# Optimization experiments

Hardware: AMD Instinct MI355X
Metric: run time of the kernel (lower is better)

## Reference

```python
import jax, jax.numpy as jnp
import numpy as np

SPARSITY_RATIO = 0.1


def setup_inputs() -> dict:
    key = jax.random.key(0)
    ks = jax.random.split(key, 11)
    B, S, d = 4, 2048, 16  # d = n_sparse_dims + 2
    inp = {
        "full": jax.random.normal(ks[0], (B, S, d), dtype=jnp.float32),
        "sw1": jax.random.normal(ks[1], (d, 32), dtype=jnp.float32) * 0.1,
        "sb1": jax.random.normal(ks[2], (32,), dtype=jnp.float32) * 0.1,
        "sw2": jax.random.normal(ks[3], (32, 1), dtype=jnp.float32) * 0.1,
        "sb2": jax.random.normal(ks[4], (1,), dtype=jnp.float32) * 0.1,
        "mw1": jax.random.normal(ks[5], (3 * d, 64), dtype=jnp.float32) * 0.1,
        "mb1": jax.random.normal(ks[6], (64,), dtype=jnp.float32) * 0.1,
        "mw2": jax.random.normal(ks[7], (64, 32), dtype=jnp.float32) * 0.1,
        "mb2": jax.random.normal(ks[8], (32,), dtype=jnp.float32) * 0.1,
        "mw3": jax.random.normal(ks[9], (32, d), dtype=jnp.float32) * 0.1,
        "mb3": jax.random.normal(ks[10], (d,), dtype=jnp.float32) * 0.1,
    }
    return inp


def reference(full, sw1, sb1, sw2, sb2, mw1, mb1, mw2, mb2, mw3, mb3):
    B, S, d = full.shape
    k = max(1, int(S * SPARSITY_RATIO))  # static python int

    # importance scores: Linear(d,32) -> ReLU -> Linear(32,1)
    scores = (jax.nn.relu(full @ sw1 + sb1) @ sw2 + sb2)[..., 0]  # [B, S]
    _, top_idx = jax.lax.top_k(scores, k)  # [B, k]

    # gather selected tokens (keys == values)
    sel = jnp.take_along_axis(full, top_idx[:, :, None], axis=1)  # [B, k, d]

    # First MLP layer on concat([q, keys, values]) decomposed to avoid the
    # [B,S,k,3d] concat: mw1 splits into query / key / value blocks.
    w_q, w_k, w_v = mw1[:d], mw1[d:2 * d], mw1[2 * d:]
    q_part = full @ w_q                     # [B, S, 64]
    kv_part = sel @ (w_k + w_v)             # [B, k, 64]
    h1 = jax.nn.relu(q_part[:, :, None, :] + kv_part[:, None, :, :] + mb1)  # [B,S,k,64]
    h2 = jax.nn.relu(h1 @ mw2 + mb2)        # [B, S, k, 32]
    out = h2 @ mw3 + mb3                    # [B, S, k, d]
    return out.mean(axis=2)                 # [B, S, d]
```

## Files before the change

kernel.cpp:

```cpp
#include <hip/hip_runtime.h>
#include <hip/hip_bf16.h>

#define BB 4
#define SS 2048
#define DD 16
#define KK 204
#define JSPLIT 8

typedef __attribute__((ext_vector_type(8))) short short8;
typedef __attribute__((ext_vector_type(4))) float f32x4;

__device__ inline short f2bf(float x) {
  __hip_bfloat16 b = __float2bfloat16(x);
  return *reinterpret_cast<short*>(&b);
}

__global__ void __launch_bounds__(128) score_kernel(
    const float* __restrict__ full, const float* __restrict__ sw1,
    const float* __restrict__ sb1, const float* __restrict__ sw2,
    const float* __restrict__ sb2, float* __restrict__ scores_g) {
  __shared__ float swT[32][16];
  __shared__ float sb1s[32], sw2s[32];
  int t = threadIdx.x;
#pragma unroll
  for (int it = 0; it < 4; it++) {
    int idx = t + it * 128;
    int n = idx & 31, k = idx >> 5;
    swT[n][k] = sw1[k * 32 + n];
  }
  if (t < 32) { sb1s[t] = sb1[t]; sw2s[t] = sw2[t]; }

  int row = blockIdx.x * 128 + t;
  const float* xp = full + row * DD;
  f32x4 x0 = *(const f32x4*)(xp);
  f32x4 x1 = *(const f32x4*)(xp + 4);
  f32x4 x2 = *(const f32x4*)(xp + 8);
  f32x4 x3 = *(const f32x4*)(xp + 12);
  __syncthreads();

  float sc = sb2[0];
#pragma unroll
  for (int n = 0; n < 32; n++) {
    const f32x4* wp = (const f32x4*)&swT[n][0];
    f32x4 w0 = wp[0], w1 = wp[1], w2 = wp[2], w3 = wp[3];
    float a = sb1s[n];
#pragma unroll
    for (int k = 0; k < 4; k++) a += x0[k] * w0[k];
#pragma unroll
    for (int k = 0; k < 4; k++) a += x1[k] * w1[k];
#pragma unroll
    for (int k = 0; k < 4; k++) a += x2[k] * w2[k];
#pragma unroll
    for (int k = 0; k < 4; k++) a += x3[k] * w3[k];
    sc += fmaxf(a, 0.f) * sw2s[n];
  }
  scores_g[row] = sc;
}

__global__ void __launch_bounds__(1024) select_kernel(
    const float* __restrict__ scores_g, int* __restrict__ s_idx_g) {
  int b = blockIdx.x;
  int t = threadIdx.x;
  int l = t & 63, w = t >> 6;

  __shared__ int hist[2048];
  __shared__ int wtot[16];
  __shared__ unsigned long long s_pfx;
  __shared__ int s_r;

  unsigned long long key[2];
#pragma unroll
  for (int e = 0; e < 2; e++) {
    int i = t + e * 1024;
    unsigned u = __float_as_uint(scores_g[b * SS + i]);
    u = (u & 0x80000000u) ? ~u : (u | 0x80000000u);
    key[e] = ((unsigned long long)u << 11) | (unsigned)(SS - 1 - i);
  }
  if (t == 0) { s_pfx = 0ull; s_r = KK; }

  for (int pass = 0; pass < 4; pass++) {
    int s = 33 - pass * 11;
    hist[t] = 0;
    hist[t + 1024] = 0;
    __syncthreads();
    unsigned long long pfx = s_pfx;
    int r = s_r;
#pragma unroll
    for (int e = 0; e < 2; e++)
      if ((key[e] >> (s + 11)) == pfx)
        atomicAdd(&hist[(int)((key[e] >> s) & 0x7FF)], 1);
    __syncthreads();
    int loc0 = hist[2 * t], loc1 = hist[2 * t + 1];
    int ls0 = loc0 + loc1, ls1 = loc1;
    int tot = ls0;
    int incl = tot;
#pragma unroll
    for (int off = 1; off < 64; off <<= 1) {
      int o = __shfl_down(incl, off);
      incl += (l + off < 64) ? o : 0;
    }
    if (l == 0) wtot[w] = incl;
    __syncthreads();
    int waveoff = 0;
    for (int ww = w + 1; ww < 16; ww++) waveoff += wtot[ww];
    int excl = waveoff + (incl - tot);
    int sufs0 = ls0 + excl, sufs1 = ls1 + excl;
    if (sufs0 >= r && sufs1 < r) {
      s_pfx = (pfx << 11) | (unsigned)(2 * t);
      s_r = r - sufs1;
    }
    if (sufs1 >= r && excl < r) {
      s_pfx = (pfx << 11) | (unsigned)(2 * t + 1);
      s_r = r - excl;
    }
    __syncthreads();
  }

  unsigned long long kstar = s_pfx;
  bool sel0 = (key[0] >= kstar), sel1 = (key[1] >= kstar);
  int c = (sel0 ? 1 : 0) + (sel1 ? 1 : 0);
  int p = c;
#pragma unroll
  for (int off = 1; off < 64; off <<= 1) {
    int o = __shfl_up(p, off);
    p += (l >= off) ? o : 0;
  }
  if (l == 63) wtot[w] = p;
  __syncthreads();
  int base = 0;
  for (int ww = 0; ww < w; ww++) base += wtot[ww];
  int pos = base + p - c;
  if (sel0) s_idx_g[b * KK + pos++] = t;
  if (sel1) s_idx_g[b * KK + pos] = t + 1024;
}

__global__ void __launch_bounds__(512) main_mfma_kernel(
    const float* __restrict__ full, const float* __restrict__ mw1,
    const float* __restrict__ mb1, const float* __restrict__ mw2,
    const float* __restrict__ mb2, const float* __restrict__ mw3,
    const float* __restrict__ mb3, const int* __restrict__ s_idx_g,
    float* __restrict__ out) {
  int mtile = blockIdx.x;
  int bs_base = mtile * 16;
  int b = bs_base >> 11;
  int t = threadIdx.x;
  int w = t >> 6;
  int l = t & 63;
  int ml = l & 15;
  int g = l >> 4;

  __shared__ float s_kvb[KK * 64];
  __shared__ float qs[16 * 64];
  __shared__ float xs[16 * 16];
  __shared__ float s_xsel[KK * DD];
  __shared__ int s_idx[KK];
  float (*red)[512] = (float(*)[512])s_kvb;

  if (t < KK) s_idx[t] = s_idx_g[b * KK + t];
  if (t < 256) xs[t] = full[bs_base * DD + t];
  __syncthreads();

  for (int i = t; i < KK * DD; i += 512)
    s_xsel[i] = full[(b * SS + s_idx[i >> 4]) * DD + (i & 15)];
  float wreg[16];
#pragma unroll
  for (int k = 0; k < 16; k++)
    wreg[k] = mw1[(16 + k) * 64 + l] + mw1[(32 + k) * 64 + l];
  float biasv = mb1[l];

  {
    int r = t >> 5, n = t & 31;
    float q0 = 0.f, q1 = 0.f;
#pragma unroll
    for (int k = 0; k < 16; k++) {
      float xv = xs[r * 16 + k];
      q0 += xv * mw1[k * 64 + n];
      q1 += xv * mw1[k * 64 + n + 32];
    }
    qs[r * 64 + n] = q0;
    qs[r * 64 + n + 32] = q1;
  }
  __syncthreads();

  for (int j = w; j < KK; j += 8) {
    const float* xr = s_xsel + j * DD;
    float a = biasv;
#pragma unroll
    for (int k = 0; k < 16; k++) a += xr[k] * wreg[k];
    s_kvb[j * 64 + l] = a;
  }

  short8 bfrag[2][2];
#pragma unroll
  for (int nt = 0; nt < 2; nt++)
#pragma unroll
    for (int kh = 0; kh < 2; kh++)
#pragma unroll
      for (int i = 0; i < 8; i++) {
        int k = kh * 32 + 8 * g + i;
        bfrag[nt][kh][i] = f2bf(mw2[k * 32 + nt * 16 + ml]);
      }
  f32x4 biasfrag[2];
#pragma unroll
  for (int nt = 0; nt < 2; nt++) {
    float bv = mb2[nt * 16 + ml];
    f32x4 bf;
    bf[0] = bv; bf[1] = bv; bf[2] = bv; bf[3] = bv;
    biasfrag[nt] = bf;
  }
  f32x4 qv[2][2];
  {
    const float* qp = qs + ml * 64 + 8 * g;
    qv[0][0] = *(const f32x4*)(qp);
    qv[0][1] = *(const f32x4*)(qp + 4);
    qv[1][0] = *(const f32x4*)(qp + 32);
    qv[1][1] = *(const f32x4*)(qp + 36);
  }
  __syncthreads();

  float accs[2][4] = {};
  int jbeg = w * 26;
  int jend = jbeg + 26;
  if (jend > KK) jend = KK;
  const float* kvbl = s_kvb + 8 * g;
#pragma unroll 2
  for (int j = jbeg; j < jend; j++) {
    const float* kp = kvbl + j * 64;
    f32x4 kv[2][2];
    kv[0][0] = *(const f32x4*)(kp);
    kv[0][1] = *(const f32x4*)(kp + 4);
    kv[1][0] = *(const f32x4*)(kp + 32);
    kv[1][1] = *(const f32x4*)(kp + 36);

    short8 afrag[2];
#pragma unroll
    for (int kh = 0; kh < 2; kh++)
#pragma unroll
      for (int hf = 0; hf < 2; hf++)
#pragma unroll
        for (int i = 0; i < 4; i++) {
          float h = fmaxf(qv[kh][hf][i] + kv[kh][hf][i], 0.f);
          afrag[kh][hf * 4 + i] = f2bf(h);
        }

#pragma unroll
    for (int nt = 0; nt < 2; nt++) {
      f32x4 c = __builtin_amdgcn_mfma_f32_16x16x32_bf16(
          afrag[0], bfrag[nt][0], biasfrag[nt], 0, 0, 0);
      c = __builtin_amdgcn_mfma_f32_16x16x32_bf16(
          afrag[1], bfrag[nt][1], c, 0, 0, 0);
#pragma unroll
      for (int r = 0; r < 4; r++) accs[nt][r] += fmaxf(c[r], 0.f);
    }
  }

  __syncthreads();
#pragma unroll
  for (int nt = 0; nt < 2; nt++)
#pragma unroll
    for (int r = 0; r < 4; r++)
      red[w][(4 * g + r) * 32 + nt * 16 + ml] = accs[nt][r];
  __syncthreads();
  float sum = 0.f;
#pragma unroll
  for (int ww = 0; ww < JSPLIT; ww++) sum += red[ww][t];
  sum *= (1.0f / (float)KK);
  red[0][t] = sum;
  __syncthreads();

  if (t < 256) {
    int m = t >> 4, dc = t & 15;
    float o = mb3[dc];
#pragma unroll
    for (int n = 0; n < 32; n++) o += red[0][m * 32 + n] * mw3[n * 16 + dc];
    out[(bs_base + m) * 16 + dc] = o;
  }
}

extern "C" void kernel_launch(void* const* d_in, const int* in_sizes, int n_in,
                              void* d_out, int out_size, void* d_ws, size_t ws_size,
                              hipStream_t stream) {
  const float* full = (const float*)d_in[0];
  const float* sw1  = (const float*)d_in[1];
  const float* sb1  = (const float*)d_in[2];
  const float* sw2  = (const float*)d_in[3];
  const float* sb2  = (const float*)d_in[4];
  const float* mw1  = (const float*)d_in[5];
  const float* mb1  = (const float*)d_in[6];
  const float* mw2  = (const float*)d_in[7];
  const float* mb2  = (const float*)d_in[8];
  const float* mw3  = (const float*)d_in[9];
  const float* mb3  = (const float*)d_in[10];
  float* out = (float*)d_out;

  float* scores_g = (float*)d_ws;
  int*   s_idx_g  = (int*)(scores_g + BB * SS);

  score_kernel<<<64, 128, 0, stream>>>(full, sw1, sb1, sw2, sb2, scores_g);
  select_kernel<<<BB, 1024, 0, stream>>>(scores_g, s_idx_g);
  main_mfma_kernel<<<BB * SS / 16, 512, 0, stream>>>(full, mw1, mb1, mw2, mb2,
                                                     mw3, mb3, s_idx_g, out);
}
```

Measured before the change: 40.89 us.

## Fuse scoring into top-k kernel and precompute key/value projections once per batch

New measurement: 47.00 us. +15.0%, slower.

```diff
diff --git a/kernel.cpp b/kernel.cpp
--- a/kernel.cpp
+++ b/kernel.cpp
@@ -15,68 +15,59 @@
   return *reinterpret_cast<short*>(&b);
 }
 
-__global__ void __launch_bounds__(128) score_kernel(
+__global__ void __launch_bounds__(1024) topk_kvb_kernel(
     const float* __restrict__ full, const float* __restrict__ sw1,
     const float* __restrict__ sb1, const float* __restrict__ sw2,
-    const float* __restrict__ sb2, float* __restrict__ scores_g) {
-  __shared__ float swT[32][16];
-  __shared__ float sb1s[32], sw2s[32];
-  int t = threadIdx.x;
-#pragma unroll
-  for (int it = 0; it < 4; it++) {
-    int idx = t + it * 128;
-    int n = idx & 31, k = idx >> 5;
-    swT[n][k] = sw1[k * 32 + n];
-  }
-  if (t < 32) { sb1s[t] = sb1[t]; sw2s[t] = sw2[t]; }
-
-  int row = blockIdx.x * 128 + t;
-  const float* xp = full + row * DD;
-  f32x4 x0 = *(const f32x4*)(xp);
-  f32x4 x1 = *(const f32x4*)(xp + 4);
-  f32x4 x2 = *(const f32x4*)(xp + 8);
-  f32x4 x3 = *(const f32x4*)(xp + 12);
-  __syncthreads();
-
-  float sc = sb2[0];
-#pragma unroll
-  for (int n = 0; n < 32; n++) {
-    const f32x4* wp = (const f32x4*)&swT[n][0];
-    f32x4 w0 = wp[0], w1 = wp[1], w2 = wp[2], w3 = wp[3];
-    float a = sb1s[n];
-#pragma unroll
-    for (int k = 0; k < 4; k++) a += x0[k] * w0[k];
-#pragma unroll
-    for (int k = 0; k < 4; k++) a += x1[k] * w1[k];
-#pragma unroll
-    for (int k = 0; k < 4; k++) a += x2[k] * w2[k];
-#pragma unroll
-    for (int k = 0; k < 4; k++) a += x3[k] * w3[k];
-    sc += fmaxf(a, 0.f) * sw2s[n];
-  }
-  scores_g[row] = sc;
-}
-
-__global__ void __launch_bounds__(1024) select_kernel(
-    const float* __restrict__ scores_g, int* __restrict__ s_idx_g) {
+    const float* __restrict__ sb2, const float* __restrict__ mw1,
+    const float* __restrict__ mb1, float* __restrict__ kvb_g) {
   int b = blockIdx.x;
   int t = threadIdx.x;
   int l = t & 63, w = t >> 6;
 
+  __shared__ float swT[32][16];
+  __shared__ float sb1s[32], sw2s[32];
   __shared__ int hist[2048];
   __shared__ int wtot[16];
   __shared__ unsigned long long s_pfx;
   __shared__ int s_r;
-
+  __shared__ int s_idx[KK];
+  __shared__ float s_x[KK * DD];
+
+  if (t < 512) { int n = t & 31, k = t >> 5; swT[n][k] = sw1[k * 32 + n]; }
+  if (t < 32) { sb1s[t] = sb1[t]; sw2s[t] = sw2[t]; }
+  if (t == 0) { s_pfx = 0ull; s_r = KK; }
+  __syncthreads();
+
+  float sb2v = sb2[0];
   unsigned long long key[2];
 #pragma unroll
   for (int e = 0; e < 2; e++) {
     int i = t + e * 1024;
-    unsigned u = __float_as_uint(scores_g[b * SS + i]);
+    const float* xp = full + (b * SS + i) * DD;
+    f32x4 x0 = *(const f32x4*)(xp);
+    f32x4 x1 = *(const f32x4*)(xp + 4);
+    f32x4 x2 = *(const f32x4*)(xp + 8);
+    f32x4 x3 = *(const f32x4*)(xp + 12);
+    float sc = sb2v;
+#pragma unroll
+    for (int n = 0; n < 32; n++) {
+      const f32x4* wp = (const f32x4*)&swT[n][0];
+      f32x4 w0 = wp[0], w1 = wp[1], w2 = wp[2], w3 = wp[3];
+      float a = sb1s[n];
+#pragma unroll
+      for (int k = 0; k < 4; k++) a += x0[k] * w0[k];
+#pragma unroll
+      for (int k = 0; k < 4; k++) a += x1[k] * w1[k];
+#pragma unroll
+      for (int k = 0; k < 4; k++) a += x2[k] * w2[k];
+#pragma unroll
+      for (int k = 0; k < 4; k++) a += x3[k] * w3[k];
+      sc += fmaxf(a, 0.f) * sw2s[n];
+    }
+    unsigned u = __float_as_uint(sc);
     u = (u & 0x80000000u) ? ~u : (u | 0x80000000u);
     key[e] = ((unsigned long long)u << 11) | (unsigned)(SS - 1 - i);
   }
-  if (t == 0) { s_pfx = 0ull; s_r = KK; }
 
   for (int pass = 0; pass < 4; pass++) {
     int s = 33 - pass * 11;
@@ -130,16 +121,32 @@
   int base = 0;
   for (int ww = 0; ww < w; ww++) base += wtot[ww];
   int pos = base + p - c;
-  if (sel0) s_idx_g[b * KK + pos++] = t;
-  if (sel1) s_idx_g[b * KK + pos] = t + 1024;
+  if (sel0) s_idx[pos++] = t;
+  if (sel1) s_idx[pos] = t + 1024;
+  __syncthreads();
+
+  for (int i = t; i < KK * DD; i += 1024)
+    s_x[i] = full[(b * SS + s_idx[i >> 4]) * DD + (i & 15)];
+  float wreg[16];
+#pragma unroll
+  for (int k = 0; k < 16; k++)
+    wreg[k] = mw1[(16 + k) * 64 + l] + mw1[(32 + k) * 64 + l];
+  float biasv = mb1[l];
+  __syncthreads();
+  for (int j = w; j < KK; j += 16) {
+    const float* xr = s_x + j * DD;
+    float a = biasv;
+#pragma unroll
+    for (int k = 0; k < 16; k++) a += xr[k] * wreg[k];
+    kvb_g[(b * KK + j) * 64 + l] = a;
+  }
 }
 
 __global__ void __launch_bounds__(512) main_mfma_kernel(
     const float* __restrict__ full, const float* __restrict__ mw1,
-    const float* __restrict__ mb1, const float* __restrict__ mw2,
-    const float* __restrict__ mb2, const float* __restrict__ mw3,
-    const float* __restrict__ mb3, const int* __restrict__ s_idx_g,
-    float* __restrict__ out) {
+    const float* __restrict__ mw2, const float* __restrict__ mb2,
+    const float* __restrict__ mw3, const float* __restrict__ mb3,
+    const float* __restrict__ kvb_g, float* __restrict__ out) {
   int mtile = blockIdx.x;
   int bs_base = mtile * 16;
   int b = bs_base >> 11;
@@ -152,21 +159,15 @@
   __shared__ float s_kvb[KK * 64];
   __shared__ float qs[16 * 64];
   __shared__ float xs[16 * 16];
-  __shared__ float s_xsel[KK * DD];
-  __shared__ int s_idx[KK];
   float (*red)[512] = (float(*)[512])s_kvb;
 
-  if (t < KK) s_idx[t] = s_idx_g[b * KK + t];
+  {
+    const f32x4* src = (const f32x4*)(kvb_g + b * KK * 64);
+    f32x4* dst = (f32x4*)s_kvb;
+    for (int i = t; i < KK * 16; i += 512) dst[i] = src[i];
+  }
   if (t < 256) xs[t] = full[bs_base * DD + t];
   __syncthreads();
-
-  for (int i = t; i < KK * DD; i += 512)
-    s_xsel[i] = full[(b * SS + s_idx[i >> 4]) * DD + (i & 15)];
-  float wreg[16];
-#pragma unroll
-  for (int k = 0; k < 16; k++)
-    wreg[k] = mw1[(16 + k) * 64 + l] + mw1[(32 + k) * 64 + l];
-  float biasv = mb1[l];
 
   {
     int r = t >> 5, n = t & 31;
@@ -179,15 +180,6 @@
     }
     qs[r * 64 + n] = q0;
     qs[r * 64 + n + 32] = q1;
-  }
-  __syncthreads();
-
-  for (int j = w; j < KK; j += 8) {
-    const float* xr = s_xsel + j * DD;
-    float a = biasv;
-#pragma unroll
-    for (int k = 0; k < 16; k++) a += xr[k] * wreg[k];
-    s_kvb[j * 64 + l] = a;
   }
 
   short8 bfrag[2][2];
@@ -208,6 +200,8 @@
     bf[0] = bv; bf[1] = bv; bf[2] = bv; bf[3] = bv;
     biasfrag[nt] = bf;
   }
+  __syncthreads();
+
   f32x4 qv[2][2];
   {
     const float* qp = qs + ml * 64 + 8 * g;
@@ -216,7 +210,6 @@
     qv[1][0] = *(const f32x4*)(qp + 32);
     qv[1][1] = *(const f32x4*)(qp + 36);
   }
-  __syncthreads();
 
   float accs[2][4] = {};
   int jbeg = w * 26;
@@ -293,11 +286,10 @@
   const float* mb3  = (const float*)d_in[10];
   float* out = (float*)d_out;
 
-  float* scores_g = (float*)d_ws;
-  int*   s_idx_g  = (int*)(scores_g + BB * SS);
-
-  score_kernel<<<64, 128, 0, stream>>>(full, sw1, sb1, sw2, sb2, scores_g);
-  select_kernel<<<BB, 1024, 0, stream>>>(scores_g, s_idx_g);
-  main_mfma_kernel<<<BB * SS / 16, 512, 0, stream>>>(full, mw1, mb1, mw2, mb2,
-                                                     mw3, mb3, s_idx_g, out);
-}
+  float* kvb_g = (float*)d_ws;
+
+  topk_kvb_kernel<<<BB, 1024, 0, stream>>>(full, sw1, sb1, sw2, sb2, mw1, mb1,
+                                           kvb_g);
+  main_mfma_kernel<<<BB * SS / 16, 512, 0, stream>>>(full, mw1, mw2, mb2, mw3,
+                                                     mb3, kvb_g, out);
+}
```

## Fuse top-k selection into main kernel, redundantly per block

Applied to the files above, without the earlier changes.

Result: faster. 38.84 us (-5.0%).

```diff
diff --git a/kernel.cpp b/kernel.cpp
--- a/kernel.cpp
+++ b/kernel.cpp
@@ -57,88 +57,11 @@
   scores_g[row] = sc;
 }
 
-__global__ void __launch_bounds__(1024) select_kernel(
-    const float* __restrict__ scores_g, int* __restrict__ s_idx_g) {
-  int b = blockIdx.x;
-  int t = threadIdx.x;
-  int l = t & 63, w = t >> 6;
-
-  __shared__ int hist[2048];
-  __shared__ int wtot[16];
-  __shared__ unsigned long long s_pfx;
-  __shared__ int s_r;
-
-  unsigned long long key[2];
-#pragma unroll
-  for (int e = 0; e < 2; e++) {
-    int i = t + e * 1024;
-    unsigned u = __float_as_uint(scores_g[b * SS + i]);
-    u = (u & 0x80000000u) ? ~u : (u | 0x80000000u);
-    key[e] = ((unsigned long long)u << 11) | (unsigned)(SS - 1 - i);
-  }
-  if (t == 0) { s_pfx = 0ull; s_r = KK; }
-
-  for (int pass = 0; pass < 4; pass++) {
-    int s = 33 - pass * 11;
-    hist[t] = 0;
-    hist[t + 1024] = 0;
-    __syncthreads();
-    unsigned long long pfx = s_pfx;
-    int r = s_r;
-#pragma unroll
-    for (int e = 0; e < 2; e++)
-      if ((key[e] >> (s + 11)) == pfx)
-        atomicAdd(&hist[(int)((key[e] >> s) & 0x7FF)], 1);
-    __syncthreads();
-    int loc0 = hist[2 * t], loc1 = hist[2 * t + 1];
-    int ls0 = loc0 + loc1, ls1 = loc1;
-    int tot = ls0;
-    int incl = tot;
-#pragma unroll
-    for (int off = 1; off < 64; off <<= 1) {
-      int o = __shfl_down(incl, off);
-      incl += (l + off < 64) ? o : 0;
-    }
-    if (l == 0) wtot[w] = incl;
-    __syncthreads();
-    int waveoff = 0;
-    for (int ww = w + 1; ww < 16; ww++) waveoff += wtot[ww];
-    int excl = waveoff + (incl - tot);
-    int sufs0 = ls0 + excl, sufs1 = ls1 + excl;
-    if (sufs0 >= r && sufs1 < r) {
-      s_pfx = (pfx << 11) | (unsigned)(2 * t);
-      s_r = r - sufs1;
-    }
-    if (sufs1 >= r && excl < r) {
-      s_pfx = (pfx << 11) | (unsigned)(2 * t + 1);
-      s_r = r - excl;
-    }
-    __syncthreads();
-  }
-
-  unsigned long long kstar = s_pfx;
-  bool sel0 = (key[0] >= kstar), sel1 = (key[1] >= kstar);
-  int c = (sel0 ? 1 : 0) + (sel1 ? 1 : 0);
-  int p = c;
-#pragma unroll
-  for (int off = 1; off < 64; off <<= 1) {
-    int o = __shfl_up(p, off);
-    p += (l >= off) ? o : 0;
-  }
-  if (l == 63) wtot[w] = p;
-  __syncthreads();
-  int base = 0;
-  for (int ww = 0; ww < w; ww++) base += wtot[ww];
-  int pos = base + p - c;
-  if (sel0) s_idx_g[b * KK + pos++] = t;
-  if (sel1) s_idx_g[b * KK + pos] = t + 1024;
-}
-
-__global__ void __launch_bounds__(512) main_mfma_kernel(
+__global__ void __launch_bounds__(512) mega_kernel(
     const float* __restrict__ full, const float* __restrict__ mw1,
     const float* __restrict__ mb1, const float* __restrict__ mw2,
     const float* __restrict__ mb2, const float* __restrict__ mw3,
-    const float* __restrict__ mb3, const int* __restrict__ s_idx_g,
+    const float* __restrict__ mb3, const float* __restrict__ scores_g,
     float* __restrict__ out) {
   int mtile = blockIdx.x;
   int bs_base = mtile * 16;
@@ -154,10 +77,86 @@
   __shared__ float xs[16 * 16];
   __shared__ float s_xsel[KK * DD];
   __shared__ int s_idx[KK];
+  __shared__ int wtot[8];
+  __shared__ unsigned long long s_pfx;
+  __shared__ int s_r;
+  int* hist = (int*)s_kvb;
   float (*red)[512] = (float(*)[512])s_kvb;
 
-  if (t < KK) s_idx[t] = s_idx_g[b * KK + t];
+  unsigned long long key[4];
+#pragma unroll
+  for (int e = 0; e < 4; e++) {
+    int i = t + e * 512;
+    unsigned u = __float_as_uint(scores_g[b * SS + i]);
+    u = (u & 0x80000000u) ? ~u : (u | 0x80000000u);
+    key[e] = ((unsigned long long)u << 11) | (unsigned)(SS - 1 - i);
+  }
   if (t < 256) xs[t] = full[bs_base * DD + t];
+  if (t == 0) { s_pfx = 0ull; s_r = KK; }
+
+  for (int pass = 0; pass < 4; pass++) {
+    int s = 33 - pass * 11;
+#pragma unroll
+    for (int z = 0; z < 4; z++) hist[t * 4 + z] = 0;
+    __syncthreads();
+    unsigned long long pfx = s_pfx;
+    int r = s_r;
+#pragma unroll
+    for (int e = 0; e < 4; e++)
+      if ((key[e] >> (s + 11)) == pfx)
+        atomicAdd(&hist[(int)((key[e] >> s) & 0x7FF)], 1);
+    __syncthreads();
+    int loc[4], ls[5];
+#pragma unroll
+    for (int i2 = 0; i2 < 4; i2++) loc[i2] = hist[t * 4 + i2];
+    ls[4] = 0;
+#pragma unroll
+    for (int i2 = 3; i2 >= 0; i2--) ls[i2] = ls[i2 + 1] + loc[i2];
+    int tot = ls[0];
+    int incl = tot;
+#pragma unroll
+    for (int off = 1; off < 64; off <<= 1) {
+      int o = __shfl_down(incl, off);
+      incl += (l + off < 64) ? o : 0;
+    }
+    if (l == 0) wtot[w] = incl;
+    __syncthreads();
+    int waveoff = 0;
+    for (int ww = w + 1; ww < 8; ww++) waveoff += wtot[ww];
+    int excl = waveoff + (incl - tot);
+#pragma unroll
+    for (int i2 = 0; i2 < 4; i2++) {
+      int sufs = ls[i2] + excl, sufn = ls[i2 + 1] + excl;
+      if (sufs >= r && sufn < r) {
+        s_pfx = (pfx << 11) | (unsigned)(t * 4 + i2);
+        s_r = r - sufn;
+      }
+    }
+    __syncthreads();
+  }
+
+  unsigned long long kstar = s_pfx;
+  bool selm[4];
+  int c = 0;
+#pragma unroll
+  for (int e = 0; e < 4; e++) {
+    selm[e] = (key[e] >= kstar);
+    c += selm[e] ? 1 : 0;
+  }
+  int p = c;
+#pragma unroll
+  for (int off = 1; off < 64; off <<= 1) {
+    int o = __shfl_up(p, off);
+    p += (l >= off) ? o : 0;
+  }
+  if (l == 63) wtot[w] = p;
+  __syncthreads();
+  int base = 0;
+  for (int ww = 0; ww < w; ww++) base += wtot[ww];
+  int pos = base + p - c;
+#pragma unroll
+  for (int e = 0; e < 4; e++)
+    if (selm[e]) s_idx[pos++] = t + e * 512;
   __syncthreads();
 
   for (int i = t; i < KK * DD; i += 512)
@@ -167,7 +166,6 @@
   for (int k = 0; k < 16; k++)
     wreg[k] = mw1[(16 + k) * 64 + l] + mw1[(32 + k) * 64 + l];
   float biasv = mb1[l];
-
   {
     int r = t >> 5, n = t & 31;
     float q0 = 0.f, q1 = 0.f;
@@ -294,10 +292,8 @@
   float* out = (float*)d_out;
 
   float* scores_g = (float*)d_ws;
-  int*   s_idx_g  = (int*)(scores_g + BB * SS);
 
   score_kernel<<<64, 128, 0, stream>>>(full, sw1, sb1, sw2, sb2, scores_g);
-  select_kernel<<<BB, 1024, 0, stream>>>(scores_g, s_idx_g);
-  main_mfma_kernel<<<BB * SS / 16, 512, 0, stream>>>(full, mw1, mb1, mw2, mb2,
-                                                     mw3, mb3, s_idx_g, out);
-}
+  mega_kernel<<<BB * SS / 16, 512, 0, stream>>>(full, mw1, mb1, mw2, mb2, mw3,
+                                                mb3, scores_g, out);
+}
```

## Fuse top-k selection into main MLP kernel with 32-row tiles

Applied to the files above, without the earlier changes.

Result: faster. 36.73 us (median of 2 runs) (-10.2%).

```diff
diff --git a/kernel.cpp b/kernel.cpp
--- a/kernel.cpp
+++ b/kernel.cpp
@@ -5,7 +5,6 @@
 #define SS 2048
 #define DD 16
 #define KK 204
-#define JSPLIT 8
 
 typedef __attribute__((ext_vector_type(8))) short short8;
 typedef __attribute__((ext_vector_type(4))) float f32x4;
@@ -57,16 +56,32 @@
   scores_g[row] = sc;
 }
 
-__global__ void __launch_bounds__(1024) select_kernel(
-    const float* __restrict__ scores_g, int* __restrict__ s_idx_g) {
-  int b = blockIdx.x;
+__global__ void __launch_bounds__(1024) mega_kernel(
+    const float* __restrict__ full, const float* __restrict__ mw1,
+    const float* __restrict__ mb1, const float* __restrict__ mw2,
+    const float* __restrict__ mb2, const float* __restrict__ mw3,
+    const float* __restrict__ mb3, const float* __restrict__ scores_g,
+    float* __restrict__ out) {
+  int bs_base = blockIdx.x * 32;
+  int b = bs_base >> 11;
   int t = threadIdx.x;
-  int l = t & 63, w = t >> 6;
-
-  __shared__ int hist[2048];
+  int w = t >> 6;
+  int l = t & 63;
+  int mt = w >> 3;
+  int wl = w & 7;
+  int ml = l & 15;
+  int g = l >> 4;
+
+  __shared__ float s_kvb[KK * 64];
+  __shared__ float qs[32 * 64];
+  __shared__ float xs[32 * 16];
+  __shared__ float s_xsel[KK * DD];
+  __shared__ int s_idx[KK];
   __shared__ int wtot[16];
   __shared__ unsigned long long s_pfx;
   __shared__ int s_r;
+  int* hist = (int*)s_kvb;
+  float (*red)[512] = (float(*)[512])s_kvb;
 
   unsigned long long key[2];
 #pragma unroll
@@ -76,7 +91,22 @@
     u = (u & 0x80000000u) ? ~u : (u | 0x80000000u);
     key[e] = ((unsigned long long)u << 11) | (unsigned)(SS - 1 - i);
   }
+  if (t < 512) xs[t] = full[bs_base * DD + t];
   if (t == 0) { s_pfx = 0ull; s_r = KK; }
+  __syncthreads();
+
+  {
+    int r = t >> 5, n = t & 31;
+    float q0 = 0.f, q1 = 0.f;
+#pragma unroll
+    for (int k = 0; k < 16; k++) {
+      float xv = xs[r * 16 + k];
+      q0 += xv * mw1[k * 64 + n];
+      q1 += xv * mw1[k * 64 + n + 32];
+    }
+    qs[r * 64 + n] = q0;
+    qs[r * 64 + n + 32] = q1;
+  }
 
   for (int pass = 0; pass < 4; pass++) {
     int s = 33 - pass * 11;
@@ -130,63 +160,36 @@
   int base = 0;
   for (int ww = 0; ww < w; ww++) base += wtot[ww];
   int pos = base + p - c;
-  if (sel0) s_idx_g[b * KK + pos++] = t;
-  if (sel1) s_idx_g[b * KK + pos] = t + 1024;
-}
-
-__global__ void __launch_bounds__(512) main_mfma_kernel(
-    const float* __restrict__ full, const float* __restrict__ mw1,
-    const float* __restrict__ mb1, const float* __restrict__ mw2,
-    const float* __restrict__ mb2, const float* __restrict__ mw3,
-    const float* __restrict__ mb3, const int* __restrict__ s_idx_g,
-    float* __restrict__ out) {
-  int mtile = blockIdx.x;
-  int bs_base = mtile * 16;
-  int b = bs_base >> 11;
-  int t = threadIdx.x;
-  int w = t >> 6;
-  int l = t & 63;
-  int ml = l & 15;
-  int g = l >> 4;
-
-  __shared__ float s_kvb[KK * 64];
-  __shared__ float qs[16 * 64];
-  __shared__ float xs[16 * 16];
-  __shared__ float s_xsel[KK * DD];
-  __shared__ int s_idx[KK];
-  float (*red)[512] = (float(*)[512])s_kvb;
-
-  if (t < KK) s_idx[t] = s_idx_g[b * KK + t];
-  if (t < 256) xs[t] = full[bs_base * DD + t];
-  __syncthreads();
-
-  for (int i = t; i < KK * DD; i += 512)
-    s_xsel[i] = full[(b * SS + s_idx[i >> 4]) * DD + (i & 15)];
+  if (sel0) s_idx[pos++] = t;
+  if (sel1) s_idx[pos] = t + 1024;
+  __syncthreads();
+
+  {
+    f32x4* dst = (f32x4*)s_xsel;
+    for (int i = t; i < KK * 4; i += 1024) {
+      int j = i >> 2, qu = i & 3;
+      dst[i] = ((const f32x4*)(full + (b * SS + s_idx[j]) * DD))[qu];
+    }
+  }
   float wreg[16];
 #pragma unroll
   for (int k = 0; k < 16; k++)
     wreg[k] = mw1[(16 + k) * 64 + l] + mw1[(32 + k) * 64 + l];
   float biasv = mb1[l];
-
-  {
-    int r = t >> 5, n = t & 31;
-    float q0 = 0.f, q1 = 0.f;
-#pragma unroll
-    for (int k = 0; k < 16; k++) {
-      float xv = xs[r * 16 + k];
-      q0 += xv * mw1[k * 64 + n];
-      q1 += xv * mw1[k * 64 + n + 32];
-    }
-    qs[r * 64 + n] = q0;
-    qs[r * 64 + n + 32] = q1;
-  }
-  __syncthreads();
-
-  for (int j = w; j < KK; j += 8) {
-    const float* xr = s_xsel + j * DD;
+  __syncthreads();
+
+  for (int j = w; j < KK; j += 16) {
+    const f32x4* xr = (const f32x4*)(s_xsel + j * DD);
+    f32x4 x0 = xr[0], x1 = xr[1], x2 = xr[2], x3 = xr[3];
     float a = biasv;
 #pragma unroll
-    for (int k = 0; k < 16; k++) a += xr[k] * wreg[k];
+    for (int k = 0; k < 4; k++) a += x0[k] * wreg[k];
+#pragma unroll
+    for (int k = 0; k < 4; k++) a += x1[k] * wreg[4 + k];
+#pragma unroll
+    for (int k = 0; k < 4; k++) a += x2[k] * wreg[8 + k];
+#pragma unroll
+    for (int k = 0; k < 4; k++) a += x3[k] * wreg[12 + k];
     s_kvb[j * 64 + l] = a;
   }
 
@@ -210,7 +213,7 @@
   }
   f32x4 qv[2][2];
   {
-    const float* qp = qs + ml * 64 + 8 * g;
+    const float* qp = qs + (mt * 16 + ml) * 64 + 8 * g;
     qv[0][0] = *(const f32x4*)(qp);
     qv[0][1] = *(const f32x4*)(qp + 4);
     qv[1][0] = *(const f32x4*)(qp + 32);
@@ -219,7 +222,7 @@
   __syncthreads();
 
   float accs[2][4] = {};
-  int jbeg = w * 26;
+  int jbeg = wl * 26;
   int jend = jbeg + 26;
   if (jend > KK) jend = KK;
   const float* kvbl = s_kvb + 8 * g;
@@ -245,12 +248,12 @@
 
 #pragma unroll
     for (int nt = 0; nt < 2; nt++) {
-      f32x4 c = __builtin_amdgcn_mfma_f32_16x16x32_bf16(
+      f32x4 cacc = __builtin_amdgcn_mfma_f32_16x16x32_bf16(
           afrag[0], bfrag[nt][0], biasfrag[nt], 0, 0, 0);
-      c = __builtin_amdgcn_mfma_f32_16x16x32_bf16(
-          afrag[1], bfrag[nt][1], c, 0, 0, 0);
-#pragma unroll
-      for (int r = 0; r < 4; r++) accs[nt][r] += fmaxf(c[r], 0.f);
+      cacc = __builtin_amdgcn_mfma_f32_16x16x32_bf16(
+          afrag[1], bfrag[nt][1], cacc, 0, 0, 0);
+#pragma unroll
+      for (int r = 0; r < 4; r++) accs[nt][r] += fmaxf(cacc[r], 0.f);
     }
   }
 
@@ -261,19 +264,23 @@
     for (int r = 0; r < 4; r++)
       red[w][(4 * g + r) * 32 + nt * 16 + ml] = accs[nt][r];
   __syncthreads();
-  float sum = 0.f;
-#pragma unroll
-  for (int ww = 0; ww < JSPLIT; ww++) sum += red[ww][t];
-  sum *= (1.0f / (float)KK);
-  red[0][t] = sum;
-  __syncthreads();
-
-  if (t < 256) {
-    int m = t >> 4, dc = t & 15;
+  {
+    int h = t >> 9, cidx = t & 511;
+    float sum = 0.f;
+#pragma unroll
+    for (int ww = 0; ww < 8; ww++) sum += red[h * 8 + ww][cidx];
+    sum *= (1.0f / (float)KK);
+    red[h * 8][cidx] = sum;
+  }
+  __syncthreads();
+
+  if (t < 512) {
+    int mt_e = t >> 8, tl = t & 255;
+    int m = tl >> 4, dc = tl & 15;
     float o = mb3[dc];
 #pragma unroll
-    for (int n = 0; n < 32; n++) o += red[0][m * 32 + n] * mw3[n * 16 + dc];
-    out[(bs_base + m) * 16 + dc] = o;
+    for (int n = 0; n < 32; n++) o += red[mt_e * 8][m * 32 + n] * mw3[n * 16 + dc];
+    out[(bs_base + mt_e * 16 + m) * 16 + dc] = o;
   }
 }
 
@@ -294,10 +301,8 @@
   float* out = (float*)d_out;
 
   float* scores_g = (float*)d_ws;
-  int*   s_idx_g  = (int*)(scores_g + BB * SS);
 
   score_kernel<<<64, 128, 0, stream>>>(full, sw1, sb1, sw2, sb2, scores_g);
-  select_kernel<<<BB, 1024, 0, stream>>>(scores_g, s_idx_g);
-  main_mfma_kernel<<<BB * SS / 16, 512, 0, stream>>>(full, mw1, mb1, mw2, mb2,
-                                                     mw3, mb3, s_idx_g, out);
+  mega_kernel<<<BB * SS / 32, 1024, 0, stream>>>(full, mw1, mb1, mw2, mb2, mw3,
+                                                 mb3, scores_g, out);
 }
```
